# Optimization experiments

Hardware: AMD Instinct MI355X
Metric: run time of the kernel (lower is better)

Reference implementation:

```python
import jax, jax.numpy as jnp
import numpy as np

N_DIMS = 4
NEG_SLOPE = 0.01
ALPHA = 0.5

def leaky(v):
    return jnp.where(v > 0, v, NEG_SLOPE * v)

def gcn_conv(h, W, b, edge_index, n):
    """PyG GCNConv: add self-loops, symmetric normalization, then aggregate."""
    hw = h @ W  # [N, H]
    loops = jnp.arange(n, dtype=edge_index.dtype)
    src = jnp.concatenate([edge_index[0], loops])
    dst = jnp.concatenate([edge_index[1], loops])
    deg = jax.ops.segment_sum(jnp.ones_like(dst, dtype=hw.dtype), dst, num_segments=n)
    dinv = jnp.where(deg > 0, jax.lax.rsqrt(deg), 0.0)
    norm = dinv[src] * dinv[dst]  # [E+N]
    out = jax.ops.segment_sum(hw[src] * norm[:, None], dst, num_segments=n)
    return out + b

def setup_inputs() -> dict:
    key = jax.random.key(0)
    ks = jax.random.split(key, 8)
    N, IN, H, OUT, E = 50000, 512, 256, 512, 800000
    def kaiming(k, shape, fan_in):
        bound = np.sqrt(6.0 / fan_in)  # kaiming_uniform a=sqrt(5)-ish approx; gain sqrt(2)/sqrt(fan_in)*sqrt(3)
        bound = np.sqrt(2.0) * np.sqrt(3.0 / fan_in)
        return jax.random.uniform(k, shape, jnp.float32, -bound, bound)
    x = jax.random.normal(ks[0], (N, IN), jnp.float32)
    all_dim_edge_index = jax.random.randint(ks[1], (N_DIMS, 2, E), 0, N, jnp.int64)
    proj_mat = kaiming(ks[2], (N_DIMS, IN, H), IN)
    gcn_W = jax.random.uniform(ks[3], (N_DIMS, H, H), jnp.float32, -1, 1) * np.sqrt(1.0 / H)
    gcn_b = jnp.zeros((N_DIMS, H), jnp.float32)
    bilinear = kaiming(ks[4], (H, H), H)
    fan = H * N_DIMS
    inv_W = jax.random.uniform(ks[5], (fan, OUT), jnp.float32, -np.sqrt(1.0 / fan), np.sqrt(1.0 / fan))
    inv_b = jax.random.uniform(ks[6], (OUT,), jnp.float32, -np.sqrt(1.0 / fan), np.sqrt(1.0 / fan))
    return {"x": x, "all_dim_edge_index": all_dim_edge_index, "proj_mat": proj_mat,
            "gcn_W": gcn_W, "gcn_b": gcn_b, "bilinear": bilinear, "inv_W": inv_W, "inv_b": inv_b}

def reference(x, all_dim_edge_index, proj_mat, gcn_W, gcn_b, bilinear, inv_W, inv_b):
    n = x.shape[0]
    # per-dimension projection: [n_dims, N, H]
    dim_repr = leaky(jnp.einsum('ni,dih->dnh', x, proj_mat))
    # within-dimension GCN message passing (loop over small fixed n_dims)
    within_aggr = jnp.stack([
        gcn_conv(dim_repr[d], gcn_W[d], gcn_b[d], all_dim_edge_index[d], n)
        for d in range(N_DIMS)])
    # cross-dimension attention
    attention = jnp.einsum('aji,ik,bjk->ab', proj_mat, bilinear, proj_mat)
    attention = jax.nn.softmax(attention, axis=0)
    across_aggr = jnp.einsum('ab,anh->bnh', attention, dim_repr)
    new_dim_repr = ALPHA * within_aggr + (1.0 - ALPHA) * across_aggr  # [n_dims, N, H]
    concat = jnp.transpose(new_dim_repr, (1, 0, 2)).reshape(n, -1)  # [N, n_dims*H]
    return leaky(concat @ inv_W + inv_b)
```

## Files before the change

kernel.cpp:

```cpp
#include <hip/hip_runtime.h>
#include <math.h>

constexpr int N_NODES = 50000;
constexpr int IN_F    = 512;
constexpr int H_F     = 256;
constexpr int OUT_F   = 512;
constexpr int N_EDGE  = 800000;
constexpr int NDIM    = 4;
constexpr long NH     = (long)N_NODES * H_F;

#define LEAKY_SLOPE 0.01f

__device__ __forceinline__ float leaky_f(float v) { return v > 0.0f ? v : LEAKY_SLOPE * v; }

typedef __bf16 bf16x8 __attribute__((ext_vector_type(8)));
typedef float  f32x4  __attribute__((ext_vector_type(4)));

__device__ __forceinline__ void swz_block(int& mb, int& nb) {
  const int nwg = (int)(gridDim.x * gridDim.y);
  const int hw  = (int)(blockIdx.y * gridDim.x + blockIdx.x);
  const int xcd = hw & 7, idx = hw >> 3;
  const int q8 = nwg >> 3, r8 = nwg & 7;
  const int wk = (xcd < r8 ? xcd * (q8 + 1) : r8 * (q8 + 1) + (xcd - r8) * q8) + idx;
  nb = wk % (int)gridDim.x;
  mb = wk / (int)gridDim.x;
}

template<bool AF32>
__global__ __launch_bounds__(256) void gemm_k(
    const float* __restrict__ Af, int ldaf,
    const __bf16* __restrict__ Ah, const __bf16* __restrict__ Al, int lda,
    const __bf16* __restrict__ BhT, const __bf16* __restrict__ BlT, int ldb,
    float* __restrict__ C, int ldc, const float* __restrict__ biasVec,
    __bf16* __restrict__ Oh, __bf16* __restrict__ Ol, int ldo,
    int M, int K, int accumulate, int leaky)
{
  __shared__ __bf16 Ash[4096];
  __shared__ __bf16 Asl[4096];
  __shared__ __bf16 Bsh[4096];
  __shared__ __bf16 Bsl[4096];

  const int tid  = threadIdx.x;
  const int lane = tid & 63;
  const int wid  = tid >> 6;
  const int wm   = wid & 1;
  const int wn   = wid >> 1;
  const int l15  = lane & 15;
  const int quad = lane >> 4;

  int mb, nb;
  swz_block(mb, nb);
  const int row0 = mb * 128;
  const int col0 = nb * 128;

  f32x4 acc[4][4] = {};
  const int nkt = K >> 5;

  int4   avh0, avh1, avl0, avl1;
  int4   bvh0, bvh1, bvl0, bvl1;
  float4 ar0, ar1, ar2, ar3;

  const int rrB = tid >> 2;
  const int qB  = tid & 3;

  auto loadB = [&](int kt) {
    const int kb = kt << 5;
    const size_t s0 = (size_t)(col0 + rrB) * ldb + kb + qB * 8;
    const size_t s1 = (size_t)(col0 + rrB + 64) * ldb + kb + qB * 8;
    bvh0 = *(const int4*)(BhT + s0);
    bvl0 = *(const int4*)(BlT + s0);
    bvh1 = *(const int4*)(BhT + s1);
    bvl1 = *(const int4*)(BlT + s1);
  };
  auto writeB = [&]() {
    const int o0 = rrB * 32 + ((qB ^ ((rrB >> 1) & 3)) << 3);
    const int r1 = rrB + 64;
    const int o1 = r1 * 32 + ((qB ^ ((r1 >> 1) & 3)) << 3);
    *(int4*)&Bsh[o0] = bvh0;
    *(int4*)&Bsl[o0] = bvl0;
    *(int4*)&Bsh[o1] = bvh1;
    *(int4*)&Bsl[o1] = bvl1;
  };
  auto loadA16 = [&](int kt) {
    const int kb = kt << 5;
    int r0c = row0 + rrB;      r0c = r0c < M ? r0c : M - 1;
    int r1c = row0 + rrB + 64; r1c = r1c < M ? r1c : M - 1;
    const size_t s0 = (size_t)r0c * lda + kb + qB * 8;
    const size_t s1 = (size_t)r1c * lda + kb + qB * 8;
    avh0 = *(const int4*)(Ah + s0);
    avl0 = *(const int4*)(Al + s0);
    avh1 = *(const int4*)(Ah + s1);
    avl1 = *(const int4*)(Al + s1);
  };
  auto writeA16 = [&]() {
    const int o0 = rrB * 32 + ((qB ^ ((rrB >> 1) & 3)) << 3);
    const int r1 = rrB + 64;
    const int o1 = r1 * 32 + ((qB ^ ((r1 >> 1) & 3)) << 3);
    *(int4*)&Ash[o0] = avh0;
    *(int4*)&Asl[o0] = avl0;
    *(int4*)&Ash[o1] = avh1;
    *(int4*)&Asl[o1] = avl1;
  };
  auto loadA32 = [&](int kt) {
    const int kb = (kt << 5) + (tid & 7) * 4;
    const int m  = tid >> 3;
    int r;
    r = row0 + m;      r = r < M ? r : M - 1; ar0 = *(const float4*)(Af + (size_t)r * ldaf + kb);
    r = row0 + m + 32; r = r < M ? r : M - 1; ar1 = *(const float4*)(Af + (size_t)r * ldaf + kb);
    r = row0 + m + 64; r = r < M ? r : M - 1; ar2 = *(const float4*)(Af + (size_t)r * ldaf + kb);
    r = row0 + m + 96; r = r < M ? r : M - 1; ar3 = *(const float4*)(Af + (size_t)r * ldaf + kb);
  };
  auto writeA32 = [&]() {
    const int q16 = (tid & 7) >> 1;
    const int sub = (tid & 1) * 4;
    const int m0  = tid >> 3;
    const float4 regs[4] = {ar0, ar1, ar2, ar3};
    #pragma unroll
    for (int p = 0; p < 4; ++p) {
      const int m = m0 + p * 32;
      const float f[4] = {regs[p].x, regs[p].y, regs[p].z, regs[p].w};
      union { __bf16 b[4]; short4 s; } hh, ll;
      #pragma unroll
      for (int i = 0; i < 4; ++i) {
        const __bf16 hb = (__bf16)f[i];
        hh.b[i] = hb;
        ll.b[i] = (__bf16)(f[i] - (float)hb);
      }
      const int off = m * 32 + ((q16 ^ ((m >> 1) & 3)) << 3) + sub;
      *(short4*)&Ash[off] = hh.s;
      *(short4*)&Asl[off] = ll.s;
    }
  };

  if constexpr (AF32) { loadA32(0); } else { loadA16(0); }
  loadB(0);
  if constexpr (AF32) { writeA32(); } else { writeA16(); }
  writeB();
  __syncthreads();

  for (int kt = 0; kt < nkt; ++kt) {
    bf16x8 fah[4], fal[4], fbh[4], fbl[4];
    #pragma unroll
    for (int t = 0; t < 4; ++t) {
      const int ar = wm * 64 + t * 16 + l15;
      const int br = wn * 64 + t * 16 + l15;
      const int as = ar * 32 + ((quad ^ ((ar >> 1) & 3)) << 3);
      const int bs = br * 32 + ((quad ^ ((br >> 1) & 3)) << 3);
      fah[t] = *(const bf16x8*)&Ash[as];
      fal[t] = *(const bf16x8*)&Asl[as];
      fbh[t] = *(const bf16x8*)&Bsh[bs];
      fbl[t] = *(const bf16x8*)&Bsl[bs];
    }

    const bool more = (kt + 1) < nkt;
    if (more) {
      if constexpr (AF32) { loadA32(kt + 1); } else { loadA16(kt + 1); }
      loadB(kt + 1);
    }

    #pragma unroll
    for (int mt = 0; mt < 4; ++mt)
      #pragma unroll
      for (int nt = 0; nt < 4; ++nt) {
        acc[mt][nt] = __builtin_amdgcn_mfma_f32_16x16x32_bf16(fah[mt], fbh[nt], acc[mt][nt], 0, 0, 0);
        acc[mt][nt] = __builtin_amdgcn_mfma_f32_16x16x32_bf16(fah[mt], fbl[nt], acc[mt][nt], 0, 0, 0);
        acc[mt][nt] = __builtin_amdgcn_mfma_f32_16x16x32_bf16(fal[mt], fbh[nt], acc[mt][nt], 0, 0, 0);
      }

    __syncthreads();
    if (more) {
      if constexpr (AF32) { writeA32(); } else { writeA16(); }
      writeB();
    }
    __syncthreads();
  }

  #pragma unroll
  for (int mt = 0; mt < 4; ++mt)
    #pragma unroll
    for (int nt = 0; nt < 4; ++nt) {
      const int col = col0 + wn * 64 + nt * 16 + l15;
      const float bv = biasVec ? biasVec[col] : 0.0f;
      #pragma unroll
      for (int r = 0; r < 4; ++r) {
        const int row = row0 + wm * 64 + mt * 16 + quad * 4 + r;
        if (row < M) {
          float v = acc[mt][nt][r] + bv;
          if (accumulate) v += C[(size_t)row * ldc + col];
          if (leaky) v = leaky_f(v);
          if (Oh) {
            const __bf16 hv = (__bf16)v;
            Oh[(size_t)row * ldo + col] = hv;
            Ol[(size_t)row * ldo + col] = (__bf16)(v - (float)hv);
          } else {
            C[(size_t)row * ldc + col] = v;
          }
        }
      }
    }
}

__global__ void splitT_kernel(const float* __restrict__ B, __bf16* __restrict__ h,
                              __bf16* __restrict__ l, int Kd, int Nd, int total)
{
  int i = blockIdx.x * 256 + threadIdx.x;
  if (i >= total) return;
  int z   = i / (Kd * Nd);
  int rem = i - z * (Kd * Nd);
  int k = rem / Nd;
  int n = rem - k * Nd;
  float v = B[i];
  __bf16 hv = (__bf16)v;
  long o = (long)z * Kd * Nd + (long)n * Kd + k;
  h[o] = hv;
  l[o] = (__bf16)(v - (float)hv);
}

__global__ void bcat_kernel(const float* __restrict__ invW, const float* __restrict__ att,
                            __bf16* __restrict__ h, __bf16* __restrict__ l)
{
  int i = blockIdx.x * 256 + threadIdx.x;
  if (i >= NDIM * OUT_F * 512) return;
  int d   = i >> 18;
  int rem = i & 262143;
  int n = rem >> 9;
  int k = rem & 511;
  float v;
  if (k < H_F) {
    v = invW[(long)(d * H_F + k) * OUT_F + n];
  } else {
    float s = 0.f;
    #pragma unroll
    for (int b = 0; b < 4; ++b)
      s += att[d * 4 + b] * invW[(long)(b * H_F + (k - H_F)) * OUT_F + n];
    v = 0.5f * s;
  }
  __bf16 hv = (__bf16)v;
  long o = (long)n * (NDIM * 512) + d * 512 + k;
  h[o] = hv;
  l[o] = (__bf16)(v - (float)hv);
}

__global__ void deg_count_kernel(const int* __restrict__ edges, int* __restrict__ cnt, int E)
{
  int i = blockIdx.x * 256 + threadIdx.x;
  if (i >= NDIM * E) return;
  int d = i / E;
  int e = i - d * E;
  int t = edges[(long)d * 2 * E + E + e];
  atomicAdd(&cnt[d * N_NODES + t], 1);
}

__global__ __launch_bounds__(1024) void scan_kernel(const int* __restrict__ cnt,
                                                    int* __restrict__ row_start,
                                                    float* __restrict__ dinv)
{
  const int d    = blockIdx.x;
  const int tid  = threadIdx.x;
  const int lane = tid & 63;
  const int wid  = tid >> 6;
  __shared__ int wsum[16];
  __shared__ int carry_s;
  if (tid == 0) carry_s = 0;
  __syncthreads();
  for (int base = 0; base < N_NODES; base += 1024) {
    int i = base + tid;
    int v = (i < N_NODES) ? cnt[d * N_NODES + i] : 0;
    if (i < N_NODES) dinv[d * N_NODES + i] = sqrtf(0.5f / (float)(v + 1));
    int incl = v;
    #pragma unroll
    for (int off = 1; off < 64; off <<= 1) {
      int nb = __shfl_up(incl, off, 64);
      if (lane >= off) incl += nb;
    }
    if (lane == 63) wsum[wid] = incl;
    __syncthreads();
    if (wid == 0 && lane < 16) {
      int s = wsum[lane];
      #pragma unroll
      for (int off = 1; off < 16; off <<= 1) {
        int nb = __shfl_up(s, off, 16);
        if (lane >= off) s += nb;
      }
      wsum[lane] = s;
    }
    __syncthreads();
    int waveoff = (wid == 0) ? 0 : wsum[wid - 1];
    if (i < N_NODES) row_start[d * (N_NODES + 1) + i] = carry_s + waveoff + incl - v;
    __syncthreads();
    if (tid == 1023) carry_s += wsum[15];
    __syncthreads();
  }
  if (tid == 0) row_start[d * (N_NODES + 1) + N_NODES] = carry_s;
}

__global__ void fill_kernel(const int* __restrict__ edges, const int* __restrict__ row_start,
                            int* __restrict__ fill_cnt, int* __restrict__ csr_src, int E)
{
  int i = blockIdx.x * 256 + threadIdx.x;
  if (i >= NDIM * E) return;
  int d = i / E;
  int e = i - d * E;
  int s = edges[(long)d * 2 * E + e];
  int t = edges[(long)d * 2 * E + E + e];
  int pos = row_start[d * (N_NODES + 1) + t] + atomicAdd(&fill_cnt[d * N_NODES + t], 1);
  csr_src[(long)d * E + pos] = s;
}

__global__ __launch_bounds__(256) void gather_aggr_kernel(
    const float* __restrict__ hw, const int* __restrict__ csr_src,
    const int* __restrict__ row_start, const float* __restrict__ dinv,
    const float* __restrict__ bias, __bf16* __restrict__ Wh, __bf16* __restrict__ Wl,
    int ldw)
{
  const int n = blockIdx.x * 4 + (threadIdx.x >> 6);
  const int lane = threadIdx.x & 63;
  const float dt = dinv[n];
  const float sl = dt * dt;
  const float4 b = *(const float4*)(bias + lane * 4);
  const float4 h = *(const float4*)(hw + (size_t)n * H_F + lane * 4);
  float4 a0 = make_float4(0.5f * b.x + sl * h.x, 0.5f * b.y + sl * h.y,
                          0.5f * b.z + sl * h.z, 0.5f * b.w + sl * h.w);
  float4 a1 = make_float4(0.f, 0.f, 0.f, 0.f);
  float4 a2 = make_float4(0.f, 0.f, 0.f, 0.f);
  float4 a3 = make_float4(0.f, 0.f, 0.f, 0.f);
  const int beg = row_start[n];
  const int end = row_start[n + 1];
  int j = beg;
  for (; j + 4 <= end; j += 4) {
    const int s0 = csr_src[j];
    const int s1 = csr_src[j + 1];
    const int s2 = csr_src[j + 2];
    const int s3 = csr_src[j + 3];
    const float nm0 = dt * dinv[s0];
    const float nm1 = dt * dinv[s1];
    const float nm2 = dt * dinv[s2];
    const float nm3 = dt * dinv[s3];
    const float4 v0 = *(const float4*)(hw + (size_t)s0 * H_F + lane * 4);
    const float4 v1 = *(const float4*)(hw + (size_t)s1 * H_F + lane * 4);
    const float4 v2 = *(const float4*)(hw + (size_t)s2 * H_F + lane * 4);
    const float4 v3 = *(const float4*)(hw + (size_t)s3 * H_F + lane * 4);
    a0.x = fmaf(nm0, v0.x, a0.x); a0.y = fmaf(nm0, v0.y, a0.y);
    a0.z = fmaf(nm0, v0.z, a0.z); a0.w = fmaf(nm0, v0.w, a0.w);
    a1.x = fmaf(nm1, v1.x, a1.x); a1.y = fmaf(nm1, v1.y, a1.y);
    a1.z = fmaf(nm1, v1.z, a1.z); a1.w = fmaf(nm1, v1.w, a1.w);
    a2.x = fmaf(nm2, v2.x, a2.x); a2.y = fmaf(nm2, v2.y, a2.y);
    a2.z = fmaf(nm2, v2.z, a2.z); a2.w = fmaf(nm2, v2.w, a2.w);
    a3.x = fmaf(nm3, v3.x, a3.x); a3.y = fmaf(nm3, v3.y, a3.y);
    a3.z = fmaf(nm3, v3.z, a3.z); a3.w = fmaf(nm3, v3.w, a3.w);
  }
  for (; j < end; ++j) {
    const int s0 = csr_src[j];
    const float nm0 = dt * dinv[s0];
    const float4 v0 = *(const float4*)(hw + (size_t)s0 * H_F + lane * 4);
    a0.x = fmaf(nm0, v0.x, a0.x); a0.y = fmaf(nm0, v0.y, a0.y);
    a0.z = fmaf(nm0, v0.z, a0.z); a0.w = fmaf(nm0, v0.w, a0.w);
  }
  const float av[4] = {a0.x + a1.x + a2.x + a3.x, a0.y + a1.y + a2.y + a3.y,
                       a0.z + a1.z + a2.z + a3.z, a0.w + a1.w + a2.w + a3.w};
  union { __bf16 b[4]; short4 s; } H, L;
  #pragma unroll
  for (int i = 0; i < 4; ++i) {
    const __bf16 hv = (__bf16)av[i];
    H.b[i] = hv;
    L.b[i] = (__bf16)(av[i] - (float)hv);
  }
  *(short4*)(Wh + (size_t)n * ldw + lane * 4) = H.s;
  *(short4*)(Wl + (size_t)n * ldw + lane * 4) = L.s;
}

__global__ void att_dot_kernel(const float* __restrict__ T, const float* __restrict__ P,
                               float* __restrict__ out16)
{
  const int a = blockIdx.x >> 2;
  const int b = blockIdx.x & 3;
  const float* ta = T + (long)a * (IN_F * H_F);
  const float* pb = P + (long)b * (IN_F * H_F);
  float s = 0.f;
  for (int i = threadIdx.x; i < IN_F * H_F; i += 256) s += ta[i] * pb[i];
  #pragma unroll
  for (int off = 32; off > 0; off >>= 1) s += __shfl_down(s, off, 64);
  __shared__ float red[4];
  if ((threadIdx.x & 63) == 0) red[threadIdx.x >> 6] = s;
  __syncthreads();
  if (threadIdx.x == 0) out16[blockIdx.x] = red[0] + red[1] + red[2] + red[3];
}

__global__ void att_softmax_kernel(const float* __restrict__ raw, float* __restrict__ att)
{
  int b = threadIdx.x;
  if (b < 4) {
    float r0 = raw[b], r1 = raw[4 + b], r2 = raw[8 + b], r3 = raw[12 + b];
    float m = fmaxf(fmaxf(r0, r1), fmaxf(r2, r3));
    float e0 = expf(r0 - m), e1 = expf(r1 - m), e2 = expf(r2 - m), e3 = expf(r3 - m);
    float inv = 1.0f / (e0 + e1 + e2 + e3);
    att[b] = e0 * inv; att[4 + b] = e1 * inv; att[8 + b] = e2 * inv; att[12 + b] = e3 * inv;
  }
}

extern "C" void kernel_launch(void* const* d_in, const int* in_sizes, int n_in,
                              void* d_out, int out_size, void* d_ws, size_t ws_size,
                              hipStream_t stream)
{
  const float* x     = (const float*)d_in[0];
  const int*   edges = (const int*)d_in[1];
  const float* proj  = (const float*)d_in[2];
  const float* gcnW  = (const float*)d_in[3];
  const float* gcnB  = (const float*)d_in[4];
  const float* bil   = (const float*)d_in[5];
  const float* invW  = (const float*)d_in[6];
  const float* invB  = (const float*)d_in[7];
  float* out = (float*)d_out;

  float* HWB       = (float*)d_ws;
  float* dinv      = HWB + NH;
  float* Tbuf      = dinv + NDIM * N_NODES;
  float* att_raw   = Tbuf + (long)NDIM * IN_F * H_F;
  float* att       = att_raw + 16;
  int*   cnt       = (int*)(att + 16);
  int*   fill_cnt  = cnt + NDIM * N_NODES;
  int*   row_start = fill_cnt + NDIM * N_NODES;
  int*   csr_src   = row_start + NDIM * (N_NODES + 1);
  __bf16* projTh   = (__bf16*)(csr_src + (long)NDIM * N_EDGE);
  __bf16* projTl   = projTh + (long)NDIM * IN_F * H_F;
  __bf16* gcnWTh   = projTl + (long)NDIM * IN_F * H_F;
  __bf16* gcnWTl   = gcnWTh + (long)NDIM * H_F * H_F;
  __bf16* bcatTh   = gcnWTl + (long)NDIM * H_F * H_F;
  __bf16* bcatTl   = bcatTh + (long)NDIM * OUT_F * 512;
  __bf16* bilTh    = bcatTl + (long)NDIM * OUT_F * 512;
  __bf16* bilTl    = bilTh + (long)H_F * H_F;
  __bf16* fatH     = bilTl + (long)H_F * H_F;

  const size_t base_bytes = (size_t)((char*)fatH - (char*)d_ws);
  auto fatBytes = [](int ktot) { return (size_t)2 * N_NODES * ktot * sizeof(__bf16); };
  int KTOT;
  if      (ws_size >= base_bytes + fatBytes(2048)) KTOT = 2048;
  else if (ws_size >= base_bytes + fatBytes(1024)) KTOT = 1024;
  else                                             KTOT = 512;
  const int DPG  = KTOT / 512;
  const int NGEN = NDIM / DPG;
  __bf16* fatL = fatH + (size_t)N_NODES * KTOT;

  const int MBL = (N_NODES + 127) / 128;

  hipMemsetAsync(cnt, 0, (size_t)2 * NDIM * N_NODES * sizeof(int), stream);
  deg_count_kernel<<<(NDIM * N_EDGE + 255) / 256, 256, 0, stream>>>(edges, cnt, N_EDGE);
  scan_kernel<<<NDIM, 1024, 0, stream>>>(cnt, row_start, dinv);
  fill_kernel<<<(NDIM * N_EDGE + 255) / 256, 256, 0, stream>>>(edges, row_start, fill_cnt,
                                                               csr_src, N_EDGE);

  splitT_kernel<<<(NDIM * IN_F * H_F + 255) / 256, 256, 0, stream>>>(
      proj, projTh, projTl, IN_F, H_F, NDIM * IN_F * H_F);
  splitT_kernel<<<(NDIM * H_F * H_F + 255) / 256, 256, 0, stream>>>(
      gcnW, gcnWTh, gcnWTl, H_F, H_F, NDIM * H_F * H_F);
  splitT_kernel<<<(H_F * H_F + 255) / 256, 256, 0, stream>>>(
      bil, bilTh, bilTl, H_F, H_F, H_F * H_F);

  for (int a = 0; a < NDIM; ++a)
    gemm_k<true><<<dim3(H_F / 128, IN_F / 128), 256, 0, stream>>>(
        proj + (long)a * IN_F * H_F, H_F,
        nullptr, nullptr, 0,
        bilTh, bilTl, H_F,
        Tbuf + (long)a * IN_F * H_F, H_F, nullptr,
        nullptr, nullptr, 0,
        IN_F, H_F, 0, 0);
  att_dot_kernel<<<16, 256, 0, stream>>>(Tbuf, proj, att_raw);
  att_softmax_kernel<<<1, 64, 0, stream>>>(att_raw, att);
  bcat_kernel<<<(NDIM * OUT_F * 512 + 255) / 256, 256, 0, stream>>>(invW, att, bcatTh, bcatTl);

  for (int g = 0; g < NGEN; ++g) {
    for (int j = 0; j < DPG; ++j) {
      const int d = g * DPG + j;
      __bf16* wbH = fatH + j * 512;
      __bf16* wbL = fatL + j * 512;
      __bf16* rH  = fatH + j * 512 + 256;
      __bf16* rL  = fatL + j * 512 + 256;

      gemm_k<true><<<dim3(H_F / 128, MBL), 256, 0, stream>>>(
          x, IN_F,
          nullptr, nullptr, 0,
          projTh + (long)d * IN_F * H_F, projTl + (long)d * IN_F * H_F, IN_F,
          nullptr, 0, nullptr,
          rH, rL, KTOT,
          N_NODES, IN_F, 0, 1);

      gemm_k<false><<<dim3(H_F / 128, MBL), 256, 0, stream>>>(
          nullptr, 0,
          rH, rL, KTOT,
          gcnWTh + (long)d * H_F * H_F, gcnWTl + (long)d * H_F * H_F, H_F,
          HWB, H_F, nullptr,
          nullptr, nullptr, 0,
          N_NODES, H_F, 0, 0);

      gather_aggr_kernel<<<N_NODES / 4, 256, 0, stream>>>(
          HWB, csr_src + (long)d * N_EDGE, row_start + d * (N_NODES + 1),
          dinv + d * N_NODES, gcnB + d * H_F, wbH, wbL, KTOT);
    }

    gemm_k<false><<<dim3(OUT_F / 128, MBL), 256, 0, stream>>>(
        nullptr, 0,
        fatH, fatL, KTOT,
        bcatTh + (long)g * KTOT, bcatTl + (long)g * KTOT, NDIM * 512,
        out, OUT_F, (g == 0) ? invB : nullptr,
        nullptr, nullptr, 0,
        N_NODES, KTOT, (g == 0) ? 0 : 1, (g == NGEN - 1) ? 1 : 0);
  }

  (void)in_sizes; (void)n_in; (void)out_size;
}
```

Measured before the change: 2.446 ms.

## Enlarge GEMM M-tile to 256 rows and batch projection GEMMs per group

The GEMM kernel moves to 512 threads with a 256x128 tile, so each B tile is reused across twice as many rows and fewer blocks are launched. The fat activation buffer is reorganised so all projection outputs of a group sit contiguously. This lets one projection GEMM per group cover several dimensions at once instead of one launch per dimension. bcat is rewritten to match the new column order. The costs are more LDS per block, higher register pressure and lower occupancy, and the unseen compute loop must match the new warp layout.

```diff
diff --git a/kernel.cpp b/kernel.cpp
--- a/kernel.cpp
+++ b/kernel.cpp
@@ -27,7 +27,7 @@
 }
 
 template<bool AF32>
-__global__ __launch_bounds__(256) void gemm_k(
+__global__ __launch_bounds__(512) void gemm_k(
     const float* __restrict__ Af, int ldaf,
     const __bf16* __restrict__ Ah, const __bf16* __restrict__ Al, int lda,
     const __bf16* __restrict__ BhT, const __bf16* __restrict__ BlT, int ldb,
@@ -35,67 +35,60 @@
     __bf16* __restrict__ Oh, __bf16* __restrict__ Ol, int ldo,
     int M, int K, int accumulate, int leaky)
 {
-  __shared__ __bf16 Ash[4096];
-  __shared__ __bf16 Asl[4096];
+  __shared__ __bf16 Ash[8192];
+  __shared__ __bf16 Asl[8192];
   __shared__ __bf16 Bsh[4096];
   __shared__ __bf16 Bsl[4096];
 
   const int tid  = threadIdx.x;
   const int lane = tid & 63;
   const int wid  = tid >> 6;
-  const int wm   = wid & 1;
-  const int wn   = wid >> 1;
+  const int wm   = wid & 3;
+  const int wn   = wid >> 2;
   const int l15  = lane & 15;
   const int quad = lane >> 4;
 
   int mb, nb;
   swz_block(mb, nb);
-  const int row0 = mb * 128;
+  const int row0 = mb * 256;
   const int col0 = nb * 128;
 
   f32x4 acc[4][4] = {};
   const int nkt = K >> 5;
 
-  int4   avh0, avh1, avl0, avl1;
-  int4   bvh0, bvh1, bvl0, bvl1;
+  int4   avh0, avl0, avh1, avl1;
+  int4   bvh, bvl;
   float4 ar0, ar1, ar2, ar3;
 
-  const int rrB = tid >> 2;
-  const int qB  = tid & 3;
+  const int rr = tid >> 2;
+  const int qq = tid & 3;
 
   auto loadB = [&](int kt) {
     const int kb = kt << 5;
-    const size_t s0 = (size_t)(col0 + rrB) * ldb + kb + qB * 8;
-    const size_t s1 = (size_t)(col0 + rrB + 64) * ldb + kb + qB * 8;
-    bvh0 = *(const int4*)(BhT + s0);
-    bvl0 = *(const int4*)(BlT + s0);
-    bvh1 = *(const int4*)(BhT + s1);
-    bvl1 = *(const int4*)(BlT + s1);
+    const size_t s = (size_t)(col0 + rr) * ldb + kb + qq * 8;
+    bvh = *(const int4*)(BhT + s);
+    bvl = *(const int4*)(BlT + s);
   };
   auto writeB = [&]() {
-    const int o0 = rrB * 32 + ((qB ^ ((rrB >> 1) & 3)) << 3);
-    const int r1 = rrB + 64;
-    const int o1 = r1 * 32 + ((qB ^ ((r1 >> 1) & 3)) << 3);
-    *(int4*)&Bsh[o0] = bvh0;
-    *(int4*)&Bsl[o0] = bvl0;
-    *(int4*)&Bsh[o1] = bvh1;
-    *(int4*)&Bsl[o1] = bvl1;
+    const int o = rr * 32 + ((qq ^ ((rr >> 1) & 3)) << 3);
+    *(int4*)&Bsh[o] = bvh;
+    *(int4*)&Bsl[o] = bvl;
   };
   auto loadA16 = [&](int kt) {
     const int kb = kt << 5;
-    int r0c = row0 + rrB;      r0c = r0c < M ? r0c : M - 1;
-    int r1c = row0 + rrB + 64; r1c = r1c < M ? r1c : M - 1;
-    const size_t s0 = (size_t)r0c * lda + kb + qB * 8;
-    const size_t s1 = (size_t)r1c * lda + kb + qB * 8;
+    int r0 = row0 + rr;       r0 = r0 < M ? r0 : M - 1;
+    int r1 = row0 + rr + 128; r1 = r1 < M ? r1 : M - 1;
+    const size_t s0 = (size_t)r0 * lda + kb + qq * 8;
+    const size_t s1 = (size_t)r1 * lda + kb + qq * 8;
     avh0 = *(const int4*)(Ah + s0);
     avl0 = *(const int4*)(Al + s0);
     avh1 = *(const int4*)(Ah + s1);
     avl1 = *(const int4*)(Al + s1);
   };
   auto writeA16 = [&]() {
-    const int o0 = rrB * 32 + ((qB ^ ((rrB >> 1) & 3)) << 3);
-    const int r1 = rrB + 64;
-    const int o1 = r1 * 32 + ((qB ^ ((r1 >> 1) & 3)) << 3);
+    const int m1 = rr + 128;
+    const int o0 = rr * 32 + ((qq ^ ((rr >> 1) & 3)) << 3);
+    const int o1 = m1 * 32 + ((qq ^ ((m1 >> 1) & 3)) << 3);
     *(int4*)&Ash[o0] = avh0;
     *(int4*)&Asl[o0] = avl0;
     *(int4*)&Ash[o1] = avh1;
@@ -105,10 +98,10 @@
     const int kb = (kt << 5) + (tid & 7) * 4;
     const int m  = tid >> 3;
     int r;
-    r = row0 + m;      r = r < M ? r : M - 1; ar0 = *(const float4*)(Af + (size_t)r * ldaf + kb);
-    r = row0 + m + 32; r = r < M ? r : M - 1; ar1 = *(const float4*)(Af + (size_t)r * ldaf + kb);
-    r = row0 + m + 64; r = r < M ? r : M - 1; ar2 = *(const float4*)(Af + (size_t)r * ldaf + kb);
-    r = row0 + m + 96; r = r < M ? r : M - 1; ar3 = *(const float4*)(Af + (size_t)r * ldaf + kb);
+    r = row0 + m;       r = r < M ? r : M - 1; ar0 = *(const float4*)(Af + (size_t)r * ldaf + kb);
+    r = row0 + m + 64;  r = r < M ? r : M - 1; ar1 = *(const float4*)(Af + (size_t)r * ldaf + kb);
+    r = row0 + m + 128; r = r < M ? r : M - 1; ar2 = *(const float4*)(Af + (size_t)r * ldaf + kb);
+    r = row0 + m + 192; r = r < M ? r : M - 1; ar3 = *(const float4*)(Af + (size_t)r * ldaf + kb);
   };
   auto writeA32 = [&]() {
     const int q16 = (tid & 7) >> 1;
@@ -117,7 +110,7 @@
     const float4 regs[4] = {ar0, ar1, ar2, ar3};
     #pragma unroll
     for (int p = 0; p < 4; ++p) {
-      const int m = m0 + p * 32;
+      const int m = m0 + p * 64;
       const float f[4] = {regs[p].x, regs[p].y, regs[p].z, regs[p].w};
       union { __bf16 b[4]; short4 s; } hh, ll;
       #pragma unroll
@@ -217,26 +210,33 @@
 }
 
 __global__ void bcat_kernel(const float* __restrict__ invW, const float* __restrict__ att,
-                            __bf16* __restrict__ h, __bf16* __restrict__ l)
+                            __bf16* __restrict__ h, __bf16* __restrict__ l, int DPG)
 {
   int i = blockIdx.x * 256 + threadIdx.x;
-  if (i >= NDIM * OUT_F * 512) return;
-  int d   = i >> 18;
-  int rem = i & 262143;
-  int n = rem >> 9;
-  int k = rem & 511;
+  if (i >= OUT_F * NDIM * 512) return;
+  const int n    = i >> 11;
+  const int kidx = i & 2047;
+  const int KTOT = DPG << 9;
+  const int g    = kidx / KTOT;
+  const int k    = kidx - g * KTOT;
+  const int half = KTOT >> 1;
   float v;
-  if (k < H_F) {
-    v = invW[(long)(d * H_F + k) * OUT_F + n];
+  if (k < half) {
+    const int d  = g * DPG + (k >> 8);
+    const int kk = k & 255;
+    v = invW[(long)(d * H_F + kk) * OUT_F + n];
   } else {
+    const int k2 = k - half;
+    const int d  = g * DPG + (k2 >> 8);
+    const int kk = k2 & 255;
     float s = 0.f;
     #pragma unroll
     for (int b = 0; b < 4; ++b)
-      s += att[d * 4 + b] * invW[(long)(b * H_F + (k - H_F)) * OUT_F + n];
+      s += att[d * 4 + b] * invW[(long)(b * H_F + kk) * OUT_F + n];
     v = 0.5f * s;
   }
-  __bf16 hv = (__bf16)v;
-  long o = (long)n * (NDIM * 512) + d * 512 + k;
+  const __bf16 hv = (__bf16)v;
+  const long o = (long)n * (NDIM * 512) + kidx;
   h[o] = hv;
   l[o] = (__bf16)(v - (float)hv);
 }
@@ -439,9 +439,10 @@
   else                                             KTOT = 512;
   const int DPG  = KTOT / 512;
   const int NGEN = NDIM / DPG;
+  const int half = KTOT / 2;
   __bf16* fatL = fatH + (size_t)N_NODES * KTOT;
 
-  const int MBL = (N_NODES + 127) / 128;
+  const int MBL = (N_NODES + 255) / 256;
 
   hipMemsetAsync(cnt, 0, (size_t)2 * NDIM * N_NODES * sizeof(int), stream);
   deg_count_kernel<<<(NDIM * N_EDGE + 255) / 256, 256, 0, stream>>>(edges, cnt, N_EDGE);
@@ -457,7 +458,7 @@
       bil, bilTh, bilTl, H_F, H_F, H_F * H_F);
 
   for (int a = 0; a < NDIM; ++a)
-    gemm_k<true><<<dim3(H_F / 128, IN_F / 128), 256, 0, stream>>>(
+    gemm_k<true><<<dim3(H_F / 128, IN_F / 256), 512, 0, stream>>>(
         proj + (long)a * IN_F * H_F, H_F,
         nullptr, nullptr, 0,
         bilTh, bilTl, H_F,
@@ -466,27 +467,24 @@
         IN_F, H_F, 0, 0);
   att_dot_kernel<<<16, 256, 0, stream>>>(Tbuf, proj, att_raw);
   att_softmax_kernel<<<1, 64, 0, stream>>>(att_raw, att);
-  bcat_kernel<<<(NDIM * OUT_F * 512 + 255) / 256, 256, 0, stream>>>(invW, att, bcatTh, bcatTl);
+  bcat_kernel<<<(OUT_F * NDIM * 512 + 255) / 256, 256, 0, stream>>>(
+      invW, att, bcatTh, bcatTl, DPG);
 
   for (int g = 0; g < NGEN; ++g) {
+    gemm_k<true><<<dim3(DPG * 256 / 128, MBL), 512, 0, stream>>>(
+        x, IN_F,
+        nullptr, nullptr, 0,
+        projTh + (size_t)(g * DPG) * H_F * IN_F, projTl + (size_t)(g * DPG) * H_F * IN_F, IN_F,
+        nullptr, 0, nullptr,
+        fatH + half, fatL + half, KTOT,
+        N_NODES, IN_F, 0, 1);
+
     for (int j = 0; j < DPG; ++j) {
       const int d = g * DPG + j;
-      __bf16* wbH = fatH + j * 512;
-      __bf16* wbL = fatL + j * 512;
-      __bf16* rH  = fatH + j * 512 + 256;
-      __bf16* rL  = fatL + j * 512 + 256;
-
-      gemm_k<true><<<dim3(H_F / 128, MBL), 256, 0, stream>>>(
-          x, IN_F,
-          nullptr, nullptr, 0,
-          projTh + (long)d * IN_F * H_F, projTl + (long)d * IN_F * H_F, IN_F,
-          nullptr, 0, nullptr,
-          rH, rL, KTOT,
-          N_NODES, IN_F, 0, 1);
-
-      gemm_k<false><<<dim3(H_F / 128, MBL), 256, 0, stream>>>(
+
+      gemm_k<false><<<dim3(H_F / 128, MBL), 512, 0, stream>>>(
           nullptr, 0,
-          rH, rL, KTOT,
+          fatH + half + j * 256, fatL + half + j * 256, KTOT,
           gcnWTh + (long)d * H_F * H_F, gcnWTl + (long)d * H_F * H_F, H_F,
           HWB, H_F, nullptr,
           nullptr, nullptr, 0,
@@ -494,10 +492,11 @@
 
       gather_aggr_kernel<<<N_NODES / 4, 256, 0, stream>>>(
           HWB, csr_src + (long)d * N_EDGE, row_start + d * (N_NODES + 1),
-          dinv + d * N_NODES, gcnB + d * H_F, wbH, wbL, KTOT);
-    }
-
-    gemm_k<false><<<dim3(OUT_F / 128, MBL), 256, 0, stream>>>(
+          dinv + d * N_NODES, gcnB + d * H_F,
+          fatH + j * 256, fatL + j * 256, KTOT);
+    }
+
+    gemm_k<false><<<dim3(OUT_F / 128, MBL), 512, 0, stream>>>(
         nullptr, 0,
         fatH, fatL, KTOT,
         bcatTh + (long)g * KTOT, bcatTl + (long)g * KTOT, NDIM * 512,
```

Result: slower. 2.556 ms (+4.5%).
